# Optimization experiments

Measured on AMD Instinct MI355X. Metric: run time of the kernel, lower is better.

The kernel has to match this reference:

```python
import jax, jax.numpy as jnp
import numpy as np

IMG = 224  # hardcoded image resolution in the original module


def setup_inputs() -> dict:
    key = jax.random.key(0)
    ks = jax.random.split(key, 6)
    b, v, n, m = 16, 8, 8192, 1024
    pc = jax.random.normal(ks[0], (b, n, 3), jnp.float32)
    # binary silhouette masks (0/1 floats), ~half zeros so many outliers exist
    mask = (jax.random.uniform(ks[1], (b, v, IMG, IMG)) < 0.5).astype(jnp.float32)
    bounds = jax.random.uniform(ks[2], (b, v, m, 2), jnp.float32) * IMG
    inv_param = jax.random.normal(ks[3], (b, v, 4, 4), jnp.float32)
    proj_fine = jax.random.uniform(ks[4], (b, v, n, 2), jnp.float32) * IMG
    proj_finez = jax.random.uniform(ks[5], (b, v, n), jnp.float32) + 0.5
    return {"pc": pc, "mask": mask, "bounds": bounds, "inv_param": inv_param,
            "proj_fine": proj_fine, "proj_finez": proj_finez, "view_id": 3}


def reference(pc, mask, bounds, inv_param, proj_fine, proj_finez, view_id):
    b = pc.shape[0]
    # --- out_distance (only view_id affects the returned pc) ---
    pxy = proj_fine[:, view_id]                                  # (b, n, 2)
    pxy = jnp.stack([pxy[..., 0], IMG - pxy[..., 1]], axis=-1)   # flip y
    pxy_i = jnp.round(pxy).astype(jnp.int32)                     # round().long()
    # ZeroPad2d(1) then index with clamp(idx+1, 0, 225)
    mv = jnp.pad(mask[:, view_id], ((0, 0), (1, 1), (1, 1)))     # (b, 226, 226)
    xi = jnp.clip(pxy_i[..., 1] + 1, 0, IMG + 1)
    yi = jnp.clip(pxy_i[..., 0] + 1, 0, IMG + 1)
    bidx = jnp.arange(b)[:, None]
    out_mask = mv[bidx, xi, yi] == 0                             # (b, n) outliers
    # K=1 KNN of (rounded) outlier pixels against boundary points, both /224
    o = pxy_i.astype(bounds.dtype) / IMG                         # (b, n, 2)
    bd = bounds[:, view_id] / IMG                                # (b, m, 2)
    d2 = ((o * o).sum(-1)[:, :, None]
          + (bd * bd).sum(-1)[:, None, :]
          - 2.0 * jnp.einsum('bnd,bmd->bnm', o, bd))             # (b, n, m)
    nn_idx = jnp.argmin(d2, axis=-1)                             # (b, n)
    # n_bound * 224 == the original boundary point, gather directly
    n_bound = jnp.take_along_axis(bounds[:, view_id], nn_idx[:, :, None], axis=1)
    # --- move_out: back-project nearest boundary point, scatter into pc ---
    z = proj_finez[:, view_id][..., None]                        # (b, n, 1)
    hom = jnp.concatenate([n_bound * z, z, jnp.ones_like(z)], axis=-1)  # (b,n,4)
    back = jnp.einsum('bnk,bkl->bnl', hom, inv_param[:, view_id])[..., :3]
    return jnp.where(out_mask[..., None], back, pc)
```

## Files before the change

### kernel.cpp

```cpp
#include <hip/hip_runtime.h>
#include <math.h>

constexpr int IMG = 224;
constexpr int Bb  = 16;
constexpr int Vv  = 8;
constexpr int Nn  = 8192;
constexpr int Mm  = 1024;
constexpr int G   = 32;
constexpr float Hh = 1.0f / 32.0f;

__global__ __launch_bounds__(256) void calib_kernel(
    const float* __restrict__ pc,
    const float* __restrict__ mask,
    const float* __restrict__ bounds,
    const float* __restrict__ inv_param,
    const float* __restrict__ proj_fine,
    const float* __restrict__ proj_finez,
    const int*   __restrict__ view_p,
    float*       __restrict__ out)
{
    const int view = *view_p;
    const int b = blockIdx.y;
    const int t = threadIdx.x;
    const int lane = t & 63;
    const int w = t >> 6;

    __shared__ float4 s_e[Mm];
    __shared__ int s_start[1025];
    __shared__ int s_cnt[1024];
    __shared__ int s_wtot[4];

    #pragma unroll
    for (int u = 0; u < 4; ++u) s_cnt[t + 256 * u] = 0;
    __syncthreads();

    const float* bnd = bounds + (size_t)(b * Vv + view) * Mm * 2;
    float bdx[4], bdy[4];
    int cell[4];
    #pragma unroll
    for (int u = 0; u < 4; ++u) {
        int j = t + 256 * u;
        float2 bxy = reinterpret_cast<const float2*>(bnd)[j];
        bdx[u] = bxy.x / (float)IMG;
        bdy[u] = bxy.y / (float)IMG;
        int cx = min(G - 1, max(0, (int)(bdx[u] * (float)G)));
        int cy = min(G - 1, max(0, (int)(bdy[u] * (float)G)));
        cell[u] = cy * G + cx;
        atomicAdd(&s_cnt[cell[u]], 1);
    }
    __syncthreads();

    int c0 = s_cnt[4 * t], c1 = s_cnt[4 * t + 1];
    int c2 = s_cnt[4 * t + 2], c3 = s_cnt[4 * t + 3];
    int psum = c0 + c1 + c2 + c3;
    int incl = psum;
    #pragma unroll
    for (int off = 1; off < 64; off <<= 1) {
        int v = __shfl_up(incl, off);
        if (lane >= off) incl += v;
    }
    if (lane == 63) s_wtot[w] = incl;
    __syncthreads();
    int basew = 0;
    for (int ww = 0; ww < w; ++ww) basew += s_wtot[ww];
    int base = basew + incl - psum;
    int st0 = base, st1 = base + c0, st2 = base + c0 + c1, st3 = base + c0 + c1 + c2;
    s_start[4 * t] = st0; s_start[4 * t + 1] = st1;
    s_start[4 * t + 2] = st2; s_start[4 * t + 3] = st3;
    if (t == 0) s_start[1024] = Mm;
    s_cnt[4 * t] = st0; s_cnt[4 * t + 1] = st1;
    s_cnt[4 * t + 2] = st2; s_cnt[4 * t + 3] = st3;
    __syncthreads();

    #pragma unroll
    for (int u = 0; u < 4; ++u) {
        int j = t + 256 * u;
        int pos = atomicAdd(&s_cnt[cell[u]], 1);
        float nrm = __fadd_rn(__fmul_rn(bdx[u], bdx[u]), __fmul_rn(bdy[u], bdy[u]));
        s_e[pos] = make_float4(bdx[u], bdy[u], nrm, __int_as_float(j));
    }
    __syncthreads();

    const int i = blockIdx.x * 256 + t;
    const size_t pf = (size_t)(b * Vv + view) * Nn + i;
    float2 pxy = reinterpret_cast<const float2*>(proj_fine)[pf];

    int i0 = (int)rintf(pxy.x);
    int i1 = (int)rintf((float)IMG - pxy.y);

    int xi = min(max(i1 + 1, 0), IMG + 1);
    int yi = min(max(i0 + 1, 0), IMG + 1);
    float mval = 0.0f;
    if (xi >= 1 && xi <= IMG && yi >= 1 && yi <= IMG)
        mval = mask[((size_t)(b * Vv + view) * IMG + (xi - 1)) * IMG + (yi - 1)];
    const bool use_back = (mval == 0.0f);

    const size_t ob = ((size_t)b * Nn + i) * 3;
    if (use_back) {
        float ox = (float)i0 / (float)IMG;
        float oy = (float)i1 / (float)IMG;
        float o2 = __fadd_rn(__fmul_rn(ox, ox), __fmul_rn(oy, oy));
        float n2ox = __fmul_rn(-2.0f, ox);
        float n2oy = __fmul_rn(-2.0f, oy);

        int cx = min(G - 1, max(0, (int)(ox * (float)G)));
        int cy = min(G - 1, max(0, (int)(oy * (float)G)));

        float best = INFINITY;
        int   bj   = 0;

        int x0 = max(cx - 2, 0), x1 = min(cx + 2, G - 1);
        int y0 = max(cy - 2, 0), y1 = min(cy + 2, G - 1);
        for (int yy = y0; yy <= y1; ++yy) {
            int rowb = yy * G;
            int e0 = s_start[rowb + x0];
            int e1 = s_start[rowb + x1 + 1];
            for (int e = e0; e < e1; ++e) {
                float4 cd = s_e[e];
                float dn = __fadd_rn(__fmul_rn(n2ox, cd.x), __fmul_rn(n2oy, cd.y));
                float d2 = __fadd_rn(__fadd_rn(o2, cd.z), dn);
                int   j  = __float_as_int(cd.w);
                bool better = (d2 < best) || (d2 == best && j < bj);
                best = better ? d2 : best;
                bj   = better ? j  : bj;
            }
        }

        if (!(best < 4.0f * Hh * Hh - 1e-5f)) {
            for (int r = 3; r <= G; ++r) {
                float lim = (float)(r - 1) * Hh;
                if (best < lim * lim - 1e-5f) break;
                int rx0 = max(0, cx - r), rx1 = min(G - 1, cx + r);
                int ry0 = max(0, cy - r), ry1 = min(G - 1, cy + r);
                for (int yy = ry0; yy <= ry1; ++yy) {
                    bool yedge = (yy == cy - r) || (yy == cy + r);
                    for (int xx = rx0; xx <= rx1; ++xx) {
                        if (!yedge && xx != cx - r && xx != cx + r) continue;
                        int c = yy * G + xx;
                        int e0 = s_start[c], e1 = s_start[c + 1];
                        for (int e = e0; e < e1; ++e) {
                            float4 cd = s_e[e];
                            float dn = __fadd_rn(__fmul_rn(n2ox, cd.x), __fmul_rn(n2oy, cd.y));
                            float d2 = __fadd_rn(__fadd_rn(o2, cd.z), dn);
                            int   j  = __float_as_int(cd.w);
                            bool better = (d2 < best) || (d2 == best && j < bj);
                            best = better ? d2 : best;
                            bj   = better ? j  : bj;
                        }
                    }
                }
            }
        }

        float nbx = bnd[2 * bj];
        float nby = bnd[2 * bj + 1];
        float z   = proj_finez[pf];
        const float* ip = inv_param + (size_t)(b * Vv + view) * 16;
        float h0 = nbx * z, h1 = nby * z;
        float r0 = h0 * ip[0] + h1 * ip[4] + z * ip[8]  + ip[12];
        float r1 = h0 * ip[1] + h1 * ip[5] + z * ip[9]  + ip[13];
        float r2 = h0 * ip[2] + h1 * ip[6] + z * ip[10] + ip[14];
        out[ob]     = r0;
        out[ob + 1] = r1;
        out[ob + 2] = r2;
    } else {
        out[ob]     = pc[ob];
        out[ob + 1] = pc[ob + 1];
        out[ob + 2] = pc[ob + 2];
    }
}

extern "C" void kernel_launch(void* const* d_in, const int* in_sizes, int n_in,
                              void* d_out, int out_size, void* d_ws, size_t ws_size,
                              hipStream_t stream) {
    const float* pc         = (const float*)d_in[0];
    const float* mask       = (const float*)d_in[1];
    const float* bounds     = (const float*)d_in[2];
    const float* inv_param  = (const float*)d_in[3];
    const float* proj_fine  = (const float*)d_in[4];
    const float* proj_finez = (const float*)d_in[5];
    const int*   view_p     = (const int*)d_in[6];
    float* out = (float*)d_out;

    dim3 grid(Nn / 256, Bb);
    calib_kernel<<<grid, 256, 0, stream>>>(pc, mask, bounds, inv_param,
                                           proj_fine, proj_finez, view_p, out);
}
```

Measured before the change: 19.05 us.

## Process two points per thread to amortize per-block grid build

```diff
diff --git a/kernel.cpp b/kernel.cpp
--- a/kernel.cpp
+++ b/kernel.cpp
@@ -64,12 +64,11 @@
     int basew = 0;
     for (int ww = 0; ww < w; ++ww) basew += s_wtot[ww];
     int base = basew + incl - psum;
-    int st0 = base, st1 = base + c0, st2 = base + c0 + c1, st3 = base + c0 + c1 + c2;
-    s_start[4 * t] = st0; s_start[4 * t + 1] = st1;
-    s_start[4 * t + 2] = st2; s_start[4 * t + 3] = st3;
+    s_start[4 * t] = base; s_start[4 * t + 1] = base + c0;
+    s_start[4 * t + 2] = base + c0 + c1; s_start[4 * t + 3] = base + c0 + c1 + c2;
     if (t == 0) s_start[1024] = Mm;
-    s_cnt[4 * t] = st0; s_cnt[4 * t + 1] = st1;
-    s_cnt[4 * t + 2] = st2; s_cnt[4 * t + 3] = st3;
+    s_cnt[4 * t] = base; s_cnt[4 * t + 1] = base + c0;
+    s_cnt[4 * t + 2] = base + c0 + c1; s_cnt[4 * t + 3] = base + c0 + c1 + c2;
     __syncthreads();
 
     #pragma unroll
@@ -81,92 +80,119 @@
     }
     __syncthreads();
 
-    const int i = blockIdx.x * 256 + t;
-    const size_t pf = (size_t)(b * Vv + view) * Nn + i;
-    float2 pxy = reinterpret_cast<const float2*>(proj_fine)[pf];
-
-    int i0 = (int)rintf(pxy.x);
-    int i1 = (int)rintf((float)IMG - pxy.y);
-
-    int xi = min(max(i1 + 1, 0), IMG + 1);
-    int yi = min(max(i0 + 1, 0), IMG + 1);
-    float mval = 0.0f;
-    if (xi >= 1 && xi <= IMG && yi >= 1 && yi <= IMG)
-        mval = mask[((size_t)(b * Vv + view) * IMG + (xi - 1)) * IMG + (yi - 1)];
-    const bool use_back = (mval == 0.0f);
-
-    const size_t ob = ((size_t)b * Nn + i) * 3;
-    if (use_back) {
-        float ox = (float)i0 / (float)IMG;
-        float oy = (float)i1 / (float)IMG;
-        float o2 = __fadd_rn(__fmul_rn(ox, ox), __fmul_rn(oy, oy));
-        float n2ox = __fmul_rn(-2.0f, ox);
-        float n2oy = __fmul_rn(-2.0f, oy);
-
-        int cx = min(G - 1, max(0, (int)(ox * (float)G)));
-        int cy = min(G - 1, max(0, (int)(oy * (float)G)));
-
-        float best = INFINITY;
-        int   bj   = 0;
-
-        int x0 = max(cx - 2, 0), x1 = min(cx + 2, G - 1);
-        int y0 = max(cy - 2, 0), y1 = min(cy + 2, G - 1);
-        for (int yy = y0; yy <= y1; ++yy) {
-            int rowb = yy * G;
-            int e0 = s_start[rowb + x0];
-            int e1 = s_start[rowb + x1 + 1];
-            for (int e = e0; e < e1; ++e) {
-                float4 cd = s_e[e];
-                float dn = __fadd_rn(__fmul_rn(n2ox, cd.x), __fmul_rn(n2oy, cd.y));
-                float d2 = __fadd_rn(__fadd_rn(o2, cd.z), dn);
-                int   j  = __float_as_int(cd.w);
-                bool better = (d2 < best) || (d2 == best && j < bj);
-                best = better ? d2 : best;
-                bj   = better ? j  : bj;
+    const int iA = blockIdx.x * 512 + t;
+    const int iB = iA + 256;
+    const size_t pbase = (size_t)(b * Vv + view) * Nn;
+    const size_t pfA = pbase + iA, pfB = pbase + iB;
+
+    float2 pxyA = reinterpret_cast<const float2*>(proj_fine)[pfA];
+    float2 pxyB = reinterpret_cast<const float2*>(proj_fine)[pfB];
+    float zA = proj_finez[pfA];
+    float zB = proj_finez[pfB];
+    const size_t obA = ((size_t)b * Nn + iA) * 3;
+    const size_t obB = ((size_t)b * Nn + iB) * 3;
+    float pcA0 = pc[obA], pcA1 = pc[obA + 1], pcA2 = pc[obA + 2];
+    float pcB0 = pc[obB], pcB1 = pc[obB + 1], pcB2 = pc[obB + 2];
+
+    int i0A = (int)rintf(pxyA.x);
+    int i1A = (int)rintf((float)IMG - pxyA.y);
+    int i0B = (int)rintf(pxyB.x);
+    int i1B = (int)rintf((float)IMG - pxyB.y);
+
+    const float* mrow = mask + (size_t)(b * Vv + view) * IMG * IMG;
+    int xiA = min(max(i1A + 1, 0), IMG + 1), yiA = min(max(i0A + 1, 0), IMG + 1);
+    int xiB = min(max(i1B + 1, 0), IMG + 1), yiB = min(max(i0B + 1, 0), IMG + 1);
+    float mvalA = 0.0f, mvalB = 0.0f;
+    if (xiA >= 1 && xiA <= IMG && yiA >= 1 && yiA <= IMG)
+        mvalA = mrow[(xiA - 1) * IMG + (yiA - 1)];
+    if (xiB >= 1 && xiB <= IMG && yiB >= 1 && yiB <= IMG)
+        mvalB = mrow[(xiB - 1) * IMG + (yiB - 1)];
+    const bool backA = (mvalA == 0.0f);
+    const bool backB = (mvalB == 0.0f);
+
+    const float* ip = inv_param + (size_t)(b * Vv + view) * 16;
+
+    #pragma unroll
+    for (int pp = 0; pp < 2; ++pp) {
+        const bool  use_back = pp ? backB : backA;
+        const int   i0 = pp ? i0B : i0A;
+        const int   i1 = pp ? i1B : i1A;
+        const float z  = pp ? zB  : zA;
+        const size_t ob = pp ? obB : obA;
+        const float c0v = pp ? pcB0 : pcA0;
+        const float c1v = pp ? pcB1 : pcA1;
+        const float c2v = pp ? pcB2 : pcA2;
+
+        if (use_back) {
+            float ox = (float)i0 / (float)IMG;
+            float oy = (float)i1 / (float)IMG;
+            float o2 = __fadd_rn(__fmul_rn(ox, ox), __fmul_rn(oy, oy));
+            float n2ox = __fmul_rn(-2.0f, ox);
+            float n2oy = __fmul_rn(-2.0f, oy);
+
+            int cx = min(G - 1, max(0, (int)(ox * (float)G)));
+            int cy = min(G - 1, max(0, (int)(oy * (float)G)));
+
+            float best = INFINITY;
+            int   bj   = 0;
+
+            int x0 = max(cx - 2, 0), x1 = min(cx + 2, G - 1);
+            int y0 = max(cy - 2, 0), y1 = min(cy + 2, G - 1);
+            for (int yy = y0; yy <= y1; ++yy) {
+                int rowb = yy * G;
+                int e0 = s_start[rowb + x0];
+                int e1 = s_start[rowb + x1 + 1];
+                for (int e = e0; e < e1; ++e) {
+                    float4 cd = s_e[e];
+                    float dn = __fadd_rn(__fmul_rn(n2ox, cd.x), __fmul_rn(n2oy, cd.y));
+                    float d2 = __fadd_rn(__fadd_rn(o2, cd.z), dn);
+                    int   j  = __float_as_int(cd.w);
+                    bool better = (d2 < best) || (d2 == best && j < bj);
+                    best = better ? d2 : best;
+                    bj   = better ? j  : bj;
+                }
             }
-        }
-
-        if (!(best < 4.0f * Hh * Hh - 1e-5f)) {
-            for (int r = 3; r <= G; ++r) {
-                float lim = (float)(r - 1) * Hh;
-                if (best < lim * lim - 1e-5f) break;
-                int rx0 = max(0, cx - r), rx1 = min(G - 1, cx + r);
-                int ry0 = max(0, cy - r), ry1 = min(G - 1, cy + r);
-                for (int yy = ry0; yy <= ry1; ++yy) {
-                    bool yedge = (yy == cy - r) || (yy == cy + r);
-                    for (int xx = rx0; xx <= rx1; ++xx) {
-                        if (!yedge && xx != cx - r && xx != cx + r) continue;
-                        int c = yy * G + xx;
-                        int e0 = s_start[c], e1 = s_start[c + 1];
-                        for (int e = e0; e < e1; ++e) {
-                            float4 cd = s_e[e];
-                            float dn = __fadd_rn(__fmul_rn(n2ox, cd.x), __fmul_rn(n2oy, cd.y));
-                            float d2 = __fadd_rn(__fadd_rn(o2, cd.z), dn);
-                            int   j  = __float_as_int(cd.w);
-                            bool better = (d2 < best) || (d2 == best && j < bj);
-                            best = better ? d2 : best;
-                            bj   = better ? j  : bj;
+
+            if (!(best < 4.0f * Hh * Hh - 1e-5f)) {
+                for (int r = 3; r <= G; ++r) {
+                    float lim = (float)(r - 1) * Hh;
+                    if (best < lim * lim - 1e-5f) break;
+                    int rx0 = max(0, cx - r), rx1 = min(G - 1, cx + r);
+                    int ry0 = max(0, cy - r), ry1 = min(G - 1, cy + r);
+                    for (int yy = ry0; yy <= ry1; ++yy) {
+                        bool yedge = (yy == cy - r) || (yy == cy + r);
+                        for (int xx = rx0; xx <= rx1; ++xx) {
+                            if (!yedge && xx != cx - r && xx != cx + r) continue;
+                            int c = yy * G + xx;
+                            int e0 = s_start[c], e1 = s_start[c + 1];
+                            for (int e = e0; e < e1; ++e) {
+                                float4 cd = s_e[e];
+                                float dn = __fadd_rn(__fmul_rn(n2ox, cd.x), __fmul_rn(n2oy, cd.y));
+                                float d2 = __fadd_rn(__fadd_rn(o2, cd.z), dn);
+                                int   j  = __float_as_int(cd.w);
+                                bool better = (d2 < best) || (d2 == best && j < bj);
+                                best = better ? d2 : best;
+                                bj   = better ? j  : bj;
+                            }
                         }
                     }
                 }
             }
+
+            float nbx = bnd[2 * bj];
+            float nby = bnd[2 * bj + 1];
+            float h0 = nbx * z, h1 = nby * z;
+            float r0 = h0 * ip[0] + h1 * ip[4] + z * ip[8]  + ip[12];
+            float r1 = h0 * ip[1] + h1 * ip[5] + z * ip[9]  + ip[13];
+            float r2 = h0 * ip[2] + h1 * ip[6] + z * ip[10] + ip[14];
+            out[ob]     = r0;
+            out[ob + 1] = r1;
+            out[ob + 2] = r2;
+        } else {
+            out[ob]     = c0v;
+            out[ob + 1] = c1v;
+            out[ob + 2] = c2v;
         }
-
-        float nbx = bnd[2 * bj];
-        float nby = bnd[2 * bj + 1];
-        float z   = proj_finez[pf];
-        const float* ip = inv_param + (size_t)(b * Vv + view) * 16;
-        float h0 = nbx * z, h1 = nby * z;
-        float r0 = h0 * ip[0] + h1 * ip[4] + z * ip[8]  + ip[12];
-        float r1 = h0 * ip[1] + h1 * ip[5] + z * ip[9]  + ip[13];
-        float r2 = h0 * ip[2] + h1 * ip[6] + z * ip[10] + ip[14];
-        out[ob]     = r0;
-        out[ob + 1] = r1;
-        out[ob + 2] = r2;
-    } else {
-        out[ob]     = pc[ob];
-        out[ob + 1] = pc[ob + 1];
-        out[ob + 2] = pc[ob + 2];
     }
 }
 
@@ -182,7 +208,7 @@
     const int*   view_p     = (const int*)d_in[6];
     float* out = (float*)d_out;
 
-    dim3 grid(Nn / 256, Bb);
+    dim3 grid(Nn / 512, Bb);
     calib_kernel<<<grid, 256, 0, stream>>>(pc, mask, bounds, inv_param,
                                            proj_fine, proj_finez, view_p, out);
 }
```

After: 24.80 us. 30.1% more time.

## Compact outlier queries into contiguous threads and overlap global loads with grid build

Applied to the files above, without the earlier changes.

```diff
diff --git a/kernel.cpp b/kernel.cpp
--- a/kernel.cpp
+++ b/kernel.cpp
@@ -29,7 +29,18 @@
     __shared__ int s_start[1025];
     __shared__ int s_cnt[1024];
     __shared__ int s_wtot[4];
-
+    __shared__ unsigned int s_qpk[256];
+    __shared__ float s_qz[256];
+    __shared__ int s_qcount;
+
+    const int ipt = blockIdx.x * 256 + t;
+    const size_t pf = (size_t)(b * Vv + view) * Nn + ipt;
+    float2 pxy = reinterpret_cast<const float2*>(proj_fine)[pf];
+    float z    = proj_finez[pf];
+    const size_t ob = ((size_t)b * Nn + ipt) * 3;
+    float pc0 = pc[ob], pc1 = pc[ob + 1], pc2 = pc[ob + 2];
+
+    if (t == 0) s_qcount = 0;
     #pragma unroll
     for (int u = 0; u < 4; ++u) s_cnt[t + 256 * u] = 0;
     __syncthreads();
@@ -48,6 +59,14 @@
         cell[u] = cy * G + cx;
         atomicAdd(&s_cnt[cell[u]], 1);
     }
+
+    int i0 = (int)rintf(pxy.x);
+    int i1 = (int)rintf((float)IMG - pxy.y);
+    int xi = min(max(i1 + 1, 0), IMG + 1);
+    int yi = min(max(i0 + 1, 0), IMG + 1);
+    float mval = 0.0f;
+    if (xi >= 1 && xi <= IMG && yi >= 1 && yi <= IMG)
+        mval = mask[((size_t)(b * Vv + view) * IMG + (xi - 1)) * IMG + (yi - 1)];
     __syncthreads();
 
     int c0 = s_cnt[4 * t], c1 = s_cnt[4 * t + 1];
@@ -64,12 +83,11 @@
     int basew = 0;
     for (int ww = 0; ww < w; ++ww) basew += s_wtot[ww];
     int base = basew + incl - psum;
-    int st0 = base, st1 = base + c0, st2 = base + c0 + c1, st3 = base + c0 + c1 + c2;
-    s_start[4 * t] = st0; s_start[4 * t + 1] = st1;
-    s_start[4 * t + 2] = st2; s_start[4 * t + 3] = st3;
+    s_start[4 * t] = base; s_start[4 * t + 1] = base + c0;
+    s_start[4 * t + 2] = base + c0 + c1; s_start[4 * t + 3] = base + c0 + c1 + c2;
     if (t == 0) s_start[1024] = Mm;
-    s_cnt[4 * t] = st0; s_cnt[4 * t + 1] = st1;
-    s_cnt[4 * t + 2] = st2; s_cnt[4 * t + 3] = st3;
+    s_cnt[4 * t] = base; s_cnt[4 * t + 1] = base + c0;
+    s_cnt[4 * t + 2] = base + c0 + c1; s_cnt[4 * t + 3] = base + c0 + c1 + c2;
     __syncthreads();
 
     #pragma unroll
@@ -79,95 +97,111 @@
         float nrm = __fadd_rn(__fmul_rn(bdx[u], bdx[u]), __fmul_rn(bdy[u], bdy[u]));
         s_e[pos] = make_float4(bdx[u], bdy[u], nrm, __int_as_float(j));
     }
-    __syncthreads();
-
-    const int i = blockIdx.x * 256 + t;
-    const size_t pf = (size_t)(b * Vv + view) * Nn + i;
-    float2 pxy = reinterpret_cast<const float2*>(proj_fine)[pf];
-
-    int i0 = (int)rintf(pxy.x);
-    int i1 = (int)rintf((float)IMG - pxy.y);
-
-    int xi = min(max(i1 + 1, 0), IMG + 1);
-    int yi = min(max(i0 + 1, 0), IMG + 1);
-    float mval = 0.0f;
-    if (xi >= 1 && xi <= IMG && yi >= 1 && yi <= IMG)
-        mval = mask[((size_t)(b * Vv + view) * IMG + (xi - 1)) * IMG + (yi - 1)];
+
     const bool use_back = (mval == 0.0f);
-
-    const size_t ob = ((size_t)b * Nn + i) * 3;
     if (use_back) {
-        float ox = (float)i0 / (float)IMG;
-        float oy = (float)i1 / (float)IMG;
-        float o2 = __fadd_rn(__fmul_rn(ox, ox), __fmul_rn(oy, oy));
-        float n2ox = __fmul_rn(-2.0f, ox);
-        float n2oy = __fmul_rn(-2.0f, oy);
-
-        int cx = min(G - 1, max(0, (int)(ox * (float)G)));
-        int cy = min(G - 1, max(0, (int)(oy * (float)G)));
-
-        float best = INFINITY;
-        int   bj   = 0;
-
-        int x0 = max(cx - 2, 0), x1 = min(cx + 2, G - 1);
-        int y0 = max(cy - 2, 0), y1 = min(cy + 2, G - 1);
-        for (int yy = y0; yy <= y1; ++yy) {
+        int pos = atomicAdd(&s_qcount, 1);
+        s_qpk[pos] = (unsigned int)t | ((unsigned int)i0 << 8)
+                   | ((unsigned int)i1 << 16);
+        s_qz[pos] = z;
+    } else {
+        out[ob]     = pc0;
+        out[ob + 1] = pc1;
+        out[ob + 2] = pc2;
+    }
+    __syncthreads();
+
+    const int qn = s_qcount;
+    if (t >= qn) return;
+
+    unsigned int pk = s_qpk[t];
+    int p  = (int)(pk & 0xFF);
+    int q0 = (int)((pk >> 8) & 0xFF);
+    int q1 = (int)((pk >> 16) & 0xFF);
+    float zq = s_qz[t];
+
+    float ox = (float)q0 / (float)IMG;
+    float oy = (float)q1 / (float)IMG;
+    float o2 = __fadd_rn(__fmul_rn(ox, ox), __fmul_rn(oy, oy));
+    float n2ox = __fmul_rn(-2.0f, ox);
+    float n2oy = __fmul_rn(-2.0f, oy);
+
+    int cx = min(G - 1, max(0, (int)(ox * (float)G)));
+    int cy = min(G - 1, max(0, (int)(oy * (float)G)));
+
+    float best = INFINITY;
+    int   bj   = 0;
+
+    int x0 = max(cx - 2, 0), x1 = min(cx + 2, G - 1);
+    int bases[5], offs[5];
+    int T = 0;
+    #pragma unroll
+    for (int r = 0; r < 5; ++r) {
+        int yy = cy - 2 + r;
+        int bb = 0, LL = 0;
+        if (yy >= 0 && yy < G) {
             int rowb = yy * G;
             int e0 = s_start[rowb + x0];
             int e1 = s_start[rowb + x1 + 1];
-            for (int e = e0; e < e1; ++e) {
-                float4 cd = s_e[e];
-                float dn = __fadd_rn(__fmul_rn(n2ox, cd.x), __fmul_rn(n2oy, cd.y));
-                float d2 = __fadd_rn(__fadd_rn(o2, cd.z), dn);
-                int   j  = __float_as_int(cd.w);
-                bool better = (d2 < best) || (d2 == best && j < bj);
-                best = better ? d2 : best;
-                bj   = better ? j  : bj;
-            }
+            bb = e0; LL = e1 - e0;
         }
-
-        if (!(best < 4.0f * Hh * Hh - 1e-5f)) {
-            for (int r = 3; r <= G; ++r) {
-                float lim = (float)(r - 1) * Hh;
-                if (best < lim * lim - 1e-5f) break;
-                int rx0 = max(0, cx - r), rx1 = min(G - 1, cx + r);
-                int ry0 = max(0, cy - r), ry1 = min(G - 1, cy + r);
-                for (int yy = ry0; yy <= ry1; ++yy) {
-                    bool yedge = (yy == cy - r) || (yy == cy + r);
-                    for (int xx = rx0; xx <= rx1; ++xx) {
-                        if (!yedge && xx != cx - r && xx != cx + r) continue;
-                        int c = yy * G + xx;
-                        int e0 = s_start[c], e1 = s_start[c + 1];
-                        for (int e = e0; e < e1; ++e) {
-                            float4 cd = s_e[e];
-                            float dn = __fadd_rn(__fmul_rn(n2ox, cd.x), __fmul_rn(n2oy, cd.y));
-                            float d2 = __fadd_rn(__fadd_rn(o2, cd.z), dn);
-                            int   j  = __float_as_int(cd.w);
-                            bool better = (d2 < best) || (d2 == best && j < bj);
-                            best = better ? d2 : best;
-                            bj   = better ? j  : bj;
-                        }
+        bases[r] = bb; offs[r] = T; T += LL;
+    }
+    for (int u = 0; u < T; ++u) {
+        int base2 = bases[0], off2 = offs[0];
+        #pragma unroll
+        for (int r = 1; r < 5; ++r) {
+            bool in = (u >= offs[r]);
+            base2 = in ? bases[r] : base2;
+            off2  = in ? offs[r]  : off2;
+        }
+        float4 cd = s_e[base2 + (u - off2)];
+        float dn = __fadd_rn(__fmul_rn(n2ox, cd.x), __fmul_rn(n2oy, cd.y));
+        float d2 = __fadd_rn(__fadd_rn(o2, cd.z), dn);
+        int   j  = __float_as_int(cd.w);
+        bool better = (d2 < best) || (d2 == best && j < bj);
+        best = better ? d2 : best;
+        bj   = better ? j  : bj;
+    }
+
+    if (!(best < 4.0f * Hh * Hh - 1e-5f)) {
+        for (int r = 3; r <= G; ++r) {
+            float lim = (float)(r - 1) * Hh;
+            if (best < lim * lim - 1e-5f) break;
+            int rx0 = max(0, cx - r), rx1 = min(G - 1, cx + r);
+            int ry0 = max(0, cy - r), ry1 = min(G - 1, cy + r);
+            for (int yy = ry0; yy <= ry1; ++yy) {
+                bool yedge = (yy == cy - r) || (yy == cy + r);
+                for (int xx = rx0; xx <= rx1; ++xx) {
+                    if (!yedge && xx != cx - r && xx != cx + r) continue;
+                    int c = yy * G + xx;
+                    int e0 = s_start[c], e1 = s_start[c + 1];
+                    for (int e = e0; e < e1; ++e) {
+                        float4 cd = s_e[e];
+                        float dn = __fadd_rn(__fmul_rn(n2ox, cd.x), __fmul_rn(n2oy, cd.y));
+                        float d2 = __fadd_rn(__fadd_rn(o2, cd.z), dn);
+                        int   j  = __float_as_int(cd.w);
+                        bool better = (d2 < best) || (d2 == best && j < bj);
+                        best = better ? d2 : best;
+                        bj   = better ? j  : bj;
                     }
                 }
             }
         }
-
-        float nbx = bnd[2 * bj];
-        float nby = bnd[2 * bj + 1];
-        float z   = proj_finez[pf];
-        const float* ip = inv_param + (size_t)(b * Vv + view) * 16;
-        float h0 = nbx * z, h1 = nby * z;
-        float r0 = h0 * ip[0] + h1 * ip[4] + z * ip[8]  + ip[12];
-        float r1 = h0 * ip[1] + h1 * ip[5] + z * ip[9]  + ip[13];
-        float r2 = h0 * ip[2] + h1 * ip[6] + z * ip[10] + ip[14];
-        out[ob]     = r0;
-        out[ob + 1] = r1;
-        out[ob + 2] = r2;
-    } else {
-        out[ob]     = pc[ob];
-        out[ob + 1] = pc[ob + 1];
-        out[ob + 2] = pc[ob + 2];
-    }
+    }
+
+    float nbx = bnd[2 * bj];
+    float nby = bnd[2 * bj + 1];
+    const float* ip = inv_param + (size_t)(b * Vv + view) * 16;
+    float h0 = nbx * zq, h1 = nby * zq;
+    float r0 = h0 * ip[0] + h1 * ip[4] + zq * ip[8]  + ip[12];
+    float r1 = h0 * ip[1] + h1 * ip[5] + zq * ip[9]  + ip[13];
+    float r2 = h0 * ip[2] + h1 * ip[6] + zq * ip[10] + ip[14];
+
+    const size_t obq = ((size_t)b * Nn + blockIdx.x * 256 + p) * 3;
+    out[obq]     = r0;
+    out[obq + 1] = r1;
+    out[obq + 2] = r2;
 }
 
 extern "C" void kernel_launch(void* const* d_in, const int* in_sizes, int n_in,
```

Result: no change. 19.07 us (+0.1%).

## Replace counting-sort grid build with fixed-capacity buckets plus overflow list

Applied to the files above, without the earlier changes.

```diff
diff --git a/kernel.cpp b/kernel.cpp
--- a/kernel.cpp
+++ b/kernel.cpp
@@ -8,6 +8,8 @@
 constexpr int Mm  = 1024;
 constexpr int G   = 32;
 constexpr float Hh = 1.0f / 32.0f;
+constexpr int CAP = 4;
+constexpr int OVF = 192;
 
 __global__ __launch_bounds__(256) void calib_kernel(
     const float* __restrict__ pc,
@@ -22,72 +24,33 @@
     const int view = *view_p;
     const int b = blockIdx.y;
     const int t = threadIdx.x;
-    const int lane = t & 63;
-    const int w = t >> 6;
 
-    __shared__ float4 s_e[Mm];
-    __shared__ int s_start[1025];
-    __shared__ int s_cnt[1024];
-    __shared__ int s_wtot[4];
+    __shared__ float2 s_xy[Mm * CAP];
+    __shared__ unsigned short s_j[Mm * CAP];
+    __shared__ int s_cnt[Mm];
+    __shared__ float2 s_oxy[OVF];
+    __shared__ unsigned short s_oj[OVF];
+    __shared__ int s_ocnt;
 
+    const float* bnd = bounds + (size_t)(b * Vv + view) * Mm * 2;
+    float2 bxy0 = reinterpret_cast<const float2*>(bnd)[t];
+    float2 bxy1 = reinterpret_cast<const float2*>(bnd)[t + 256];
+    float2 bxy2 = reinterpret_cast<const float2*>(bnd)[t + 512];
+    float2 bxy3 = reinterpret_cast<const float2*>(bnd)[t + 768];
+
+    const int ipt = blockIdx.x * 256 + t;
+    const size_t pf = (size_t)(b * Vv + view) * Nn + ipt;
+    float2 pxy = reinterpret_cast<const float2*>(proj_fine)[pf];
+    float z    = proj_finez[pf];
+    const size_t ob = ((size_t)b * Nn + ipt) * 3;
+    float pc0 = pc[ob], pc1 = pc[ob + 1], pc2 = pc[ob + 2];
+
+    if (t == 0) s_ocnt = 0;
     #pragma unroll
     for (int u = 0; u < 4; ++u) s_cnt[t + 256 * u] = 0;
-    __syncthreads();
-
-    const float* bnd = bounds + (size_t)(b * Vv + view) * Mm * 2;
-    float bdx[4], bdy[4];
-    int cell[4];
-    #pragma unroll
-    for (int u = 0; u < 4; ++u) {
-        int j = t + 256 * u;
-        float2 bxy = reinterpret_cast<const float2*>(bnd)[j];
-        bdx[u] = bxy.x / (float)IMG;
-        bdy[u] = bxy.y / (float)IMG;
-        int cx = min(G - 1, max(0, (int)(bdx[u] * (float)G)));
-        int cy = min(G - 1, max(0, (int)(bdy[u] * (float)G)));
-        cell[u] = cy * G + cx;
-        atomicAdd(&s_cnt[cell[u]], 1);
-    }
-    __syncthreads();
-
-    int c0 = s_cnt[4 * t], c1 = s_cnt[4 * t + 1];
-    int c2 = s_cnt[4 * t + 2], c3 = s_cnt[4 * t + 3];
-    int psum = c0 + c1 + c2 + c3;
-    int incl = psum;
-    #pragma unroll
-    for (int off = 1; off < 64; off <<= 1) {
-        int v = __shfl_up(incl, off);
-        if (lane >= off) incl += v;
-    }
-    if (lane == 63) s_wtot[w] = incl;
-    __syncthreads();
-    int basew = 0;
-    for (int ww = 0; ww < w; ++ww) basew += s_wtot[ww];
-    int base = basew + incl - psum;
-    int st0 = base, st1 = base + c0, st2 = base + c0 + c1, st3 = base + c0 + c1 + c2;
-    s_start[4 * t] = st0; s_start[4 * t + 1] = st1;
-    s_start[4 * t + 2] = st2; s_start[4 * t + 3] = st3;
-    if (t == 0) s_start[1024] = Mm;
-    s_cnt[4 * t] = st0; s_cnt[4 * t + 1] = st1;
-    s_cnt[4 * t + 2] = st2; s_cnt[4 * t + 3] = st3;
-    __syncthreads();
-
-    #pragma unroll
-    for (int u = 0; u < 4; ++u) {
-        int j = t + 256 * u;
-        int pos = atomicAdd(&s_cnt[cell[u]], 1);
-        float nrm = __fadd_rn(__fmul_rn(bdx[u], bdx[u]), __fmul_rn(bdy[u], bdy[u]));
-        s_e[pos] = make_float4(bdx[u], bdy[u], nrm, __int_as_float(j));
-    }
-    __syncthreads();
-
-    const int i = blockIdx.x * 256 + t;
-    const size_t pf = (size_t)(b * Vv + view) * Nn + i;
-    float2 pxy = reinterpret_cast<const float2*>(proj_fine)[pf];
 
     int i0 = (int)rintf(pxy.x);
     int i1 = (int)rintf((float)IMG - pxy.y);
-
     int xi = min(max(i1 + 1, 0), IMG + 1);
     int yi = min(max(i0 + 1, 0), IMG + 1);
     float mval = 0.0f;
@@ -95,79 +58,110 @@
         mval = mask[((size_t)(b * Vv + view) * IMG + (xi - 1)) * IMG + (yi - 1)];
     const bool use_back = (mval == 0.0f);
 
-    const size_t ob = ((size_t)b * Nn + i) * 3;
-    if (use_back) {
-        float ox = (float)i0 / (float)IMG;
-        float oy = (float)i1 / (float)IMG;
-        float o2 = __fadd_rn(__fmul_rn(ox, ox), __fmul_rn(oy, oy));
-        float n2ox = __fmul_rn(-2.0f, ox);
-        float n2oy = __fmul_rn(-2.0f, oy);
+    __syncthreads();
 
-        int cx = min(G - 1, max(0, (int)(ox * (float)G)));
-        int cy = min(G - 1, max(0, (int)(oy * (float)G)));
+    {
+        float2 ba[4] = {bxy0, bxy1, bxy2, bxy3};
+        #pragma unroll
+        for (int u = 0; u < 4; ++u) {
+            int j = t + 256 * u;
+            float bdx = ba[u].x / (float)IMG;
+            float bdy = ba[u].y / (float)IMG;
+            int cx = min(G - 1, max(0, (int)(bdx * (float)G)));
+            int cy = min(G - 1, max(0, (int)(bdy * (float)G)));
+            int c  = cy * G + cx;
+            int slot = atomicAdd(&s_cnt[c], 1);
+            if (slot < CAP) {
+                s_xy[c * CAP + slot] = make_float2(bdx, bdy);
+                s_j [c * CAP + slot] = (unsigned short)j;
+            } else {
+                int op = atomicAdd(&s_ocnt, 1);
+                s_oxy[op] = make_float2(bdx, bdy);
+                s_oj [op] = (unsigned short)j;
+            }
+        }
+    }
 
-        float best = INFINITY;
-        int   bj   = 0;
+    if (!use_back) {
+        out[ob]     = pc0;
+        out[ob + 1] = pc1;
+        out[ob + 2] = pc2;
+    }
+    __syncthreads();
 
+    if (!use_back) return;
+
+    float ox = (float)i0 / (float)IMG;
+    float oy = (float)i1 / (float)IMG;
+    float o2 = __fadd_rn(__fmul_rn(ox, ox), __fmul_rn(oy, oy));
+    float n2ox = __fmul_rn(-2.0f, ox);
+    float n2oy = __fmul_rn(-2.0f, oy);
+
+    int cx = min(G - 1, max(0, (int)(ox * (float)G)));
+    int cy = min(G - 1, max(0, (int)(oy * (float)G)));
+
+    float best = INFINITY;
+    int   bj   = 0;
+
+    #define EVAL_SLOT(XY, JJ)                                               \
+    {                                                                       \
+        float bdx_ = (XY).x, bdy_ = (XY).y;                                 \
+        float nrm_ = __fadd_rn(__fmul_rn(bdx_, bdx_), __fmul_rn(bdy_, bdy_)); \
+        float dn_  = __fadd_rn(__fmul_rn(n2ox, bdx_), __fmul_rn(n2oy, bdy_)); \
+        float d2_  = __fadd_rn(__fadd_rn(o2, nrm_), dn_);                   \
+        int   j_   = (int)(JJ);                                             \
+        bool better_ = (d2_ < best) || (d2_ == best && j_ < bj);            \
+        best = better_ ? d2_ : best;                                        \
+        bj   = better_ ? j_  : bj;                                          \
+    }
+
+    {
         int x0 = max(cx - 2, 0), x1 = min(cx + 2, G - 1);
         int y0 = max(cy - 2, 0), y1 = min(cy + 2, G - 1);
         for (int yy = y0; yy <= y1; ++yy) {
-            int rowb = yy * G;
-            int e0 = s_start[rowb + x0];
-            int e1 = s_start[rowb + x1 + 1];
-            for (int e = e0; e < e1; ++e) {
-                float4 cd = s_e[e];
-                float dn = __fadd_rn(__fmul_rn(n2ox, cd.x), __fmul_rn(n2oy, cd.y));
-                float d2 = __fadd_rn(__fadd_rn(o2, cd.z), dn);
-                int   j  = __float_as_int(cd.w);
-                bool better = (d2 < best) || (d2 == best && j < bj);
-                best = better ? d2 : best;
-                bj   = better ? j  : bj;
+            for (int xx = x0; xx <= x1; ++xx) {
+                int c = yy * G + xx;
+                int n = min(s_cnt[c], CAP);
+                int bs = c * CAP;
+                for (int s = 0; s < n; ++s) EVAL_SLOT(s_xy[bs + s], s_j[bs + s]);
             }
         }
+    }
+    {
+        int on = s_ocnt;
+        for (int e = 0; e < on; ++e) EVAL_SLOT(s_oxy[e], s_oj[e]);
+    }
 
-        if (!(best < 4.0f * Hh * Hh - 1e-5f)) {
-            for (int r = 3; r <= G; ++r) {
-                float lim = (float)(r - 1) * Hh;
-                if (best < lim * lim - 1e-5f) break;
-                int rx0 = max(0, cx - r), rx1 = min(G - 1, cx + r);
-                int ry0 = max(0, cy - r), ry1 = min(G - 1, cy + r);
-                for (int yy = ry0; yy <= ry1; ++yy) {
-                    bool yedge = (yy == cy - r) || (yy == cy + r);
-                    for (int xx = rx0; xx <= rx1; ++xx) {
-                        if (!yedge && xx != cx - r && xx != cx + r) continue;
-                        int c = yy * G + xx;
-                        int e0 = s_start[c], e1 = s_start[c + 1];
-                        for (int e = e0; e < e1; ++e) {
-                            float4 cd = s_e[e];
-                            float dn = __fadd_rn(__fmul_rn(n2ox, cd.x), __fmul_rn(n2oy, cd.y));
-                            float d2 = __fadd_rn(__fadd_rn(o2, cd.z), dn);
-                            int   j  = __float_as_int(cd.w);
-                            bool better = (d2 < best) || (d2 == best && j < bj);
-                            best = better ? d2 : best;
-                            bj   = better ? j  : bj;
-                        }
-                    }
+    if (!(best < 4.0f * Hh * Hh - 1e-5f)) {
+        for (int r = 3; r <= G; ++r) {
+            float lim = (float)(r - 1) * Hh;
+            if (best < lim * lim - 1e-5f) break;
+            int rx0 = max(0, cx - r), rx1 = min(G - 1, cx + r);
+            int ry0 = max(0, cy - r), ry1 = min(G - 1, cy + r);
+            for (int yy = ry0; yy <= ry1; ++yy) {
+                bool yedge = (yy == cy - r) || (yy == cy + r);
+                for (int xx = rx0; xx <= rx1; ++xx) {
+                    if (!yedge && xx != cx - r && xx != cx + r) continue;
+                    int c = yy * G + xx;
+                    int n = min(s_cnt[c], CAP);
+                    int bs = c * CAP;
+                    for (int s = 0; s < n; ++s) EVAL_SLOT(s_xy[bs + s], s_j[bs + s]);
                 }
             }
         }
+    }
+    #undef EVAL_SLOT
 
-        float nbx = bnd[2 * bj];
-        float nby = bnd[2 * bj + 1];
-        float z   = proj_finez[pf];
-        const float* ip = inv_param + (size_t)(b * Vv + view) * 16;
-        float h0 = nbx * z, h1 = nby * z;
-        float r0 = h0 * ip[0] + h1 * ip[4] + z * ip[8]  + ip[12];
-        float r1 = h0 * ip[1] + h1 * ip[5] + z * ip[9]  + ip[13];
-        float r2 = h0 * ip[2] + h1 * ip[6] + z * ip[10] + ip[14];
-        out[ob]     = r0;
-        out[ob + 1] = r1;
-        out[ob + 2] = r2;
-    } else {
-        out[ob]     = pc[ob];
-        out[ob + 1] = pc[ob + 1];
-        out[ob + 2] = pc[ob + 2];
-    }
+    float nbx = bnd[2 * bj];
+    float nby = bnd[2 * bj + 1];
+    const float* ip = inv_param + (size_t)(b * Vv + view) * 16;
+    float h0 = nbx * z, h1 = nby * z;
+    float r0 = h0 * ip[0] + h1 * ip[4] + z * ip[8]  + ip[12];
+    float r1 = h0 * ip[1] + h1 * ip[5] + z * ip[9]  + ip[13];
+    float r2 = h0 * ip[2] + h1 * ip[6] + z * ip[10] + ip[14];
+    out[ob]     = r0;
+    out[ob + 1] = r1;
+    out[ob + 2] = r2;
 }
 
 extern "C" void kernel_launch(void* const* d_in, const int* in_sizes, int n_in,
```

Result: slower. 25.84 us (+35.6%).
